# Optimization experiments

Measured on AMD Instinct MI355X. Metric: run time of the kernel, lower is better.

Reference implementation:

```python
import jax, jax.numpy as jnp
import numpy as np

D_IN = 1024
D_OUT = 1024
N_HEADS = 16

def setup_inputs() -> dict:
    key = jax.random.key(0)
    ks = jax.random.split(key, 6)
    s = 0.02
    return {
        "x": jax.random.normal(ks[0], (4, 2048, D_IN), dtype=jnp.float32),
        "Wq": jax.random.normal(ks[1], (D_IN, D_OUT), dtype=jnp.float32) * s,
        "Wk": jax.random.normal(ks[2], (D_IN, D_OUT), dtype=jnp.float32) * s,
        "Wv": jax.random.normal(ks[3], (D_IN, D_OUT), dtype=jnp.float32) * s,
        "Wo": jax.random.normal(ks[4], (D_OUT, D_OUT), dtype=jnp.float32) * s,
        "bo": jax.random.normal(ks[5], (D_OUT,), dtype=jnp.float32) * s,
    }

def reference(x, Wq, Wk, Wv, Wo, bo):
    b, n, _ = x.shape
    hd = D_OUT // N_HEADS
    # project and split heads -> [b, h, n, hd]
    def split(t):
        return t.reshape(b, n, N_HEADS, hd).transpose(0, 2, 1, 3)
    q = split(x @ Wq)
    k = split(x @ Wk)
    v = split(x @ Wv)
    scores = jnp.einsum('bhqd,bhkd->bhqk', q, k)  # [b,h,n,n]
    causal = jnp.tril(jnp.ones((n, n), dtype=bool))
    scores = jnp.where(causal, scores, -jnp.inf)
    attn = jax.nn.softmax(scores / jnp.sqrt(jnp.float32(hd)), axis=-1)
    ctx = jnp.einsum('bhqk,bhkd->bhqd', attn, v)  # [b,h,n,hd]
    ctx = ctx.transpose(0, 2, 1, 3).reshape(b, n, D_OUT)
    return ctx @ Wo + bo
```

## Files before the change

### kernel.cpp

```cpp
#include <hip/hip_runtime.h>
#include <stdint.h>

typedef unsigned short u16;
typedef __attribute__((ext_vector_type(8))) short frag8;
typedef __attribute__((ext_vector_type(4))) float f32x4;
typedef __attribute__((ext_vector_type(4))) unsigned short u16x4;
typedef __attribute__((ext_vector_type(2))) unsigned int u32x2;

#define MFMA_BF16(a,b,c) __builtin_amdgcn_mfma_f32_16x16x32_bf16((a),(b),(c),0,0,0)
#define SMSCALE 0.18033688011112042f
#define EXP2R(x) __builtin_amdgcn_exp2f(x)

__device__ __forceinline__ u16 f2bf(float f) {
  union { float f; uint32_t u; } c; c.f = f;
  uint32_t u = c.u;
  uint32_t r = (u + 0x7fffu + ((u >> 16) & 1u)) >> 16;
  return (u16)r;
}

__device__ __forceinline__ uint32_t pack_bf16(float a, float b) {
  uint32_t au = __float_as_uint(a) + 0x8000u;
  uint32_t bu = __float_as_uint(b) + 0x8000u;
  return __builtin_amdgcn_perm(bu, au, 0x07060302u);
}
__device__ __forceinline__ uint32_t pack_bf16_trunc(float a, float b) {
  return __builtin_amdgcn_perm(__float_as_uint(b), __float_as_uint(a), 0x07060302u);
}

__device__ __forceinline__ void async16(const void* g, void* l) {
  __builtin_amdgcn_global_load_lds((const __attribute__((address_space(1))) void*)g,
                                   (__attribute__((address_space(3))) void*)l,
                                   16, 0, 0);
}

__global__ __launch_bounds__(256) void k_prep(
    const float4* __restrict__ x, u16* __restrict__ xb,
    const float* __restrict__ W0, const float* __restrict__ W1,
    const float* __restrict__ W2, const float* __restrict__ W3,
    u16* __restrict__ D0, u16* __restrict__ D1,
    u16* __restrict__ D2, u16* __restrict__ D3) {
  __shared__ float tile[64][65];
  if (blockIdx.x < 8192) {
    int i = blockIdx.x * 256 + threadIdx.x;
    float4 v = x[i];
    u16x4 o;
    o.x = f2bf(v.x); o.y = f2bf(v.y); o.z = f2bf(v.z); o.w = f2bf(v.w);
    *(u16x4*)(xb + (size_t)i * 4) = o;
    return;
  }
  const int id = blockIdx.x - 8192;
  const int z = id & 3;
  const float* src = (z == 0) ? W0 : (z == 1) ? W1 : (z == 2) ? W2 : W3;
  u16* dst = (z == 0) ? D0 : (z == 1) ? D1 : (z == 2) ? D2 : D3;
  const int bx = ((id >> 2) & 15) * 64;
  const int by = (id >> 6) * 64;
  const int t = threadIdx.x;
  const int tc = (t & 15) * 4;
  const int tr = t >> 4;
  #pragma unroll
  for (int p = 0; p < 4; ++p) {
    int r = tr + p * 16;
    float4 v = *(const float4*)(src + (size_t)(bx + r) * 1024 + by + tc);
    tile[r][tc + 0] = v.x; tile[r][tc + 1] = v.y;
    tile[r][tc + 2] = v.z; tile[r][tc + 3] = v.w;
  }
  __syncthreads();
  #pragma unroll
  for (int p = 0; p < 4; ++p) {
    int r = tr + p * 16;
    u16x4 o;
    o.x = f2bf(tile[tc + 0][r]);
    o.y = f2bf(tile[tc + 1][r]);
    o.z = f2bf(tile[tc + 2][r]);
    o.w = f2bf(tile[tc + 3][r]);
    *(u16x4*)(dst + (size_t)(by + r) * 1024 + bx + tc) = o;
  }
}

__global__ __launch_bounds__(256, 2) void k_gemm_qkv(const u16* __restrict__ xb,
    const u16* __restrict__ Wqt, const u16* __restrict__ Wkt, const u16* __restrict__ Wvt,
    u16* __restrict__ Qg, u16* __restrict__ Kg, u16* __restrict__ Vtg) {
  __shared__ __attribute__((aligned(16))) u16 smem[4 * 128 * 64];
  u16* T = smem;
  const int m0 = blockIdx.x * 128, n0 = blockIdx.y * 128;
  const int t = threadIdx.x, lane = t & 63, wv = t >> 6;
  const int lm = lane & 15, quad = lane >> 4;
  const int wr = wv >> 1, wc = wv & 1;
  f32x4 acc[3][4][4] = {};

  for (int k0 = 0; k0 < 1024; k0 += 64) {
    #pragma unroll
    for (int it = 0; it < 4; ++it) {
      int chunk = it * 256 + t;
      int r = chunk >> 3;
      int sc = ((chunk & 7) ^ (r & 7)) * 8;
      async16(xb + (size_t)(m0 + r) * 1024 + k0 + sc,
              smem + (size_t)(it * 256 + wv * 64) * 8);
    }
    #pragma unroll
    for (int z = 0; z < 3; ++z) {
      const u16* Bt = (z == 0) ? Wqt : (z == 1) ? Wkt : Wvt;
      #pragma unroll
      for (int it = 0; it < 4; ++it) {
        int chunk = it * 256 + t;
        int r = chunk >> 3;
        int sc = ((chunk & 7) ^ (r & 7)) * 8;
        async16(Bt + (size_t)(n0 + r) * 1024 + k0 + sc,
                smem + (size_t)((z + 1) * 1024 + it * 256 + wv * 64) * 8);
      }
    }
    __syncthreads();
    #pragma unroll
    for (int kk = 0; kk < 2; ++kk) {
      frag8 a[4];
      #pragma unroll
      for (int i = 0; i < 4; ++i) {
        int row = wr * 64 + i * 16 + lm;
        a[i] = *(const frag8*)(smem + row * 64 + (((kk * 4 + quad) ^ (row & 7)) * 8));
      }
      #pragma unroll
      for (int z = 0; z < 3; ++z) {
        #pragma unroll
        for (int j = 0; j < 4; ++j) {
          int row = wc * 64 + j * 16 + lm;
          frag8 b = *(const frag8*)(smem + (z + 1) * 8192 + row * 64 +
                                    (((kk * 4 + quad) ^ (row & 7)) * 8));
          #pragma unroll
          for (int i = 0; i < 4; ++i)
            acc[z][i][j] = MFMA_BF16(a[i], b, acc[z][i][j]);
        }
      }
    }
    __syncthreads();
  }

  #pragma unroll
  for (int z = 0; z < 2; ++z) {
    u16* tgt = z ? Kg : Qg;
    const float sc = z ? 1.0f : SMSCALE;
    #pragma unroll
    for (int i = 0; i < 4; ++i)
      #pragma unroll
      for (int j = 0; j < 4; ++j) {
        const int col = n0 + wc * 64 + j * 16 + lm;
        const int h = col >> 6, d = col & 63;
        #pragma unroll
        for (int reg = 0; reg < 4; ++reg) {
          const int row = m0 + wr * 64 + i * 16 + quad * 4 + reg;
          const int bb = row >> 11, nn = row & 2047;
          tgt[(((size_t)bb * 16 + h) * 2048 + nn) * 64 + d] = f2bf(acc[z][i][j][reg] * sc);
        }
      }
  }
  {
    const int bb = m0 >> 11, nn0 = m0 & 2047;
    const int h0 = n0 >> 6;
    #pragma unroll
    for (int p = 0; p < 2; ++p) {
      if (wc == p) {
        #pragma unroll
        for (int i = 0; i < 4; ++i)
          #pragma unroll
          for (int j = 0; j < 4; ++j) {
            const int rT = j * 16 + lm;
            #pragma unroll
            for (int reg = 0; reg < 4; ++reg) {
              const int cT = wr * 64 + i * 16 + quad * 4 + reg;
              T[rT * 136 + cT] = f2bf(acc[2][i][j][reg]);
            }
          }
      }
      __syncthreads();
      #pragma unroll
      for (int cc = 0; cc < 4; ++cc) {
        int chunk = cc * 256 + t;
        int r = chunk >> 4, tk = (chunk & 15) * 8;
        frag8 v = *(const frag8*)(T + r * 136 + tk);
        *(frag8*)(Vtg + (((size_t)bb * 16 + h0 + p) * 64 + r) * 2048 + nn0 + tk) = v;
      }
      __syncthreads();
    }
  }
}

__global__ __launch_bounds__(256, 2) void k_attn(const u16* __restrict__ Qg,
                                                 const u16* __restrict__ Kg,
                                                 const u16* __restrict__ Vtg,
                                                 u16* __restrict__ ctx) {
  __shared__ __attribute__((aligned(16))) u16 Ks[2][64 * 64];
  __shared__ __attribute__((aligned(16))) u16 Vts[2][64 * 64];
  __shared__ __attribute__((aligned(16))) u16 Ps[4 * 16 * 72];
  const int bid = blockIdx.x;
  const int ib = bid >> 6;
  const int bh = ((bid >> 3) & 7) * 8 + (bid & 7);
  const int qts[4] = {2 * ib, 2 * ib + 1, 30 - 2 * ib, 31 - 2 * ib};
  const int t = threadIdx.x, lane = t & 63, wv = t >> 6;
  const int lm = lane & 15, quad = lane >> 4;
  const int b = bh >> 4, h = bh & 15;
  u16* const PsW = Ps + wv * (16 * 72);

  frag8 aq[4][2];
  #pragma unroll
  for (int qa = 0; qa < 4; ++qa) {
    const u16* qp = Qg + ((size_t)bh * 2048 + qts[qa] * 64 + wv * 16 + lm) * 64 + quad * 8;
    aq[qa][0] = *(const frag8*)(qp);
    aq[qa][1] = *(const frag8*)(qp + 32);
  }
  f32x4 o[4][4] = {};
  float l[4] = {0.f, 0.f, 0.f, 0.f};
  const int nst = 32 - 2 * ib;

  const u16* ksrc[2]; const u16* vsrc[2];
  #pragma unroll
  for (int it = 0; it < 2; ++it) {
    int chunk = it * 256 + t;
    int r = chunk >> 3, c = chunk & 7;
    int sc = (c ^ (r & 7)) * 8;
    ksrc[it] = Kg  + ((size_t)bh * 2048 + r) * 64 + sc;
    vsrc[it] = Vtg + ((size_t)bh * 64 + r) * 2048 + sc;
  }
  int offs[8];
  #pragma unroll
  for (int x = 0; x < 4; ++x)
    #pragma unroll
    for (int y = 0; y < 2; ++y)
      offs[x * 2 + y] = (x * 16 + lm) * 64 + (((y * 4 + quad) ^ (lm & 7)) * 8);

  auto stage = [&](int kt, int buf) {
    #pragma unroll
    for (int it = 0; it < 2; ++it) {
      async16(ksrc[it] + (size_t)kt * 4096, &Ks[buf][(it * 256 + wv * 64) * 8]);
      async16(vsrc[it] + (size_t)kt * 64,   &Vts[buf][(it * 256 + wv * 64) * 8]);
    }
  };

  stage(0, 0);
  for (int kt0 = 0; kt0 < nst; ++kt0) {
    const int cur = kt0 & 1;
    __syncthreads();
    if (kt0 + 1 < nst) stage(kt0 + 1, cur ^ 1);

    frag8 kf[8];
    #pragma unroll
    for (int i = 0; i < 8; ++i) kf[i] = *(const frag8*)(&Ks[cur][offs[i]]);

    uint32_t pk[4][8];
    #pragma unroll
    for (int qa = 0; qa < 4; ++qa) {
      if (qts[qa] < kt0) continue;
      f32x4 s[4];
      #pragma unroll
      for (int kt = 0; kt < 4; ++kt) {
        f32x4 z = {0.f, 0.f, 0.f, 0.f};
        z = MFMA_BF16(kf[kt * 2 + 0], aq[qa][0], z);
        z = MFMA_BF16(kf[kt * 2 + 1], aq[qa][1], z);
        s[kt] = z;
      }
      if (kt0 == qts[qa]) {
        #pragma unroll
        for (int kt = 0; kt < 4; ++kt)
          #pragma unroll
          for (int rg = 0; rg < 4; ++rg)
            if (kt * 16 + quad * 4 + rg > wv * 16 + lm) s[kt][rg] = -3.0e38f;
      }
      float rs = 0.f;
      #pragma unroll
      for (int kt = 0; kt < 4; ++kt) {
        float p0 = EXP2R(s[kt][0]);
        float p1 = EXP2R(s[kt][1]);
        float p2 = EXP2R(s[kt][2]);
        float p3 = EXP2R(s[kt][3]);
        rs += (p0 + p1) + (p2 + p3);
        pk[qa][kt * 2 + 0] = pack_bf16_trunc(p0, p1);
        pk[qa][kt * 2 + 1] = pack_bf16_trunc(p2, p3);
      }
      l[qa] += rs;
    }

    frag8 vf[8];
    #pragma unroll
    for (int i = 0; i < 8; ++i) vf[i] = *(const frag8*)(&Vts[cur][offs[i]]);

    #pragma unroll
    for (int qa = 0; qa < 4; ++qa) {
      if (qts[qa] < kt0) continue;
      #pragma unroll
      for (int kt = 0; kt < 4; ++kt) {
        u32x2 w; w.x = pk[qa][kt * 2 + 0]; w.y = pk[qa][kt * 2 + 1];
        *(u32x2*)(PsW + lm * 72 + kt * 16 + quad * 4) = w;
      }
      #pragma unroll
      for (int ks = 0; ks < 2; ++ks) {
        frag8 bp = *(const frag8*)(PsW + lm * 72 + ks * 32 + quad * 8);
        #pragma unroll
        for (int dt = 0; dt < 4; ++dt)
          o[qa][dt] = MFMA_BF16(vf[dt * 2 + ks], bp, o[qa][dt]);
      }
    }
  }

  #pragma unroll
  for (int qa = 0; qa < 4; ++qa) {
    float lv = l[qa];
    lv += __shfl_xor(lv, 16);
    lv += __shfl_xor(lv, 32);
    const float inv = 1.0f / lv;
    #pragma unroll
    for (int dt = 0; dt < 4; ++dt) {
      *(uint32_t*)(PsW + lm * 72 + dt * 16 + quad * 4)     = pack_bf16(o[qa][dt][0] * inv, o[qa][dt][1] * inv);
      *(uint32_t*)(PsW + lm * 72 + dt * 16 + quad * 4 + 2) = pack_bf16(o[qa][dt][2] * inv, o[qa][dt][3] * inv);
    }
    const int rr = lane >> 2, cc = (lane & 3) * 8;
    const size_t row = (size_t)b * 2048 + qts[qa] * 64 + wv * 16 + rr;
    #pragma unroll
    for (int half = 0; half < 2; ++half) {
      frag8 vo = *(const frag8*)(PsW + rr * 72 + cc + half * 32);
      *(frag8*)(ctx + row * 1024 + h * 64 + cc + half * 32) = vo;
    }
  }
}

__global__ __launch_bounds__(256) void k_gemm_out(const u16* __restrict__ ctx,
    const u16* __restrict__ Wot, const float* __restrict__ bo, float* __restrict__ out) {
  __shared__ __attribute__((aligned(16))) u16 As[128 * 64];
  __shared__ __attribute__((aligned(16))) u16 Bs[128 * 64];
  const int m0 = blockIdx.x * 128, n0 = blockIdx.y * 128;
  const int t = threadIdx.x, lane = t & 63, wv = t >> 6;
  const int lm = lane & 15, quad = lane >> 4;
  const int wr = wv >> 1, wc = wv & 1;
  f32x4 acc[4][4] = {};
  for (int k0 = 0; k0 < 1024; k0 += 64) {
    #pragma unroll
    for (int it = 0; it < 4; ++it) {
      int chunk = it * 256 + t;
      int r = chunk >> 3;
      int sc = ((chunk & 7) ^ (r & 7)) * 8;
      async16(ctx + (size_t)(m0 + r) * 1024 + k0 + sc, As + (size_t)(it * 256 + wv * 64) * 8);
      async16(Wot + (size_t)(n0 + r) * 1024 + k0 + sc, Bs + (size_t)(it * 256 + wv * 64) * 8);
    }
    __syncthreads();
    #pragma unroll
    for (int kk = 0; kk < 2; ++kk) {
      frag8 a[4];
      #pragma unroll
      for (int i = 0; i < 4; ++i) {
        int row = wr * 64 + i * 16 + lm;
        a[i] = *(const frag8*)(As + row * 64 + (((kk * 4 + quad) ^ (row & 7)) * 8));
      }
      #pragma unroll
      for (int j = 0; j < 4; ++j) {
        int row = wc * 64 + j * 16 + lm;
        frag8 b = *(const frag8*)(Bs + row * 64 + (((kk * 4 + quad) ^ (row & 7)) * 8));
        #pragma unroll
        for (int i = 0; i < 4; ++i)
          acc[i][j] = MFMA_BF16(a[i], b, acc[i][j]);
      }
    }
    __syncthreads();
  }
  #pragma unroll
  for (int i = 0; i < 4; ++i)
    #pragma unroll
    for (int j = 0; j < 4; ++j) {
      const int col = n0 + wc * 64 + j * 16 + lm;
      const float bias = bo[col];
      #pragma unroll
      for (int reg = 0; reg < 4; ++reg) {
        const int row = m0 + wr * 64 + i * 16 + quad * 4 + reg;
        out[(size_t)row * 1024 + col] = acc[i][j][reg] + bias;
      }
    }
}

extern "C" void kernel_launch(void* const* d_in, const int* in_sizes, int n_in,
                              void* d_out, int out_size, void* d_ws, size_t ws_size,
                              hipStream_t stream) {
  const float* x  = (const float*)d_in[0];
  const float* Wq = (const float*)d_in[1];
  const float* Wk = (const float*)d_in[2];
  const float* Wv = (const float*)d_in[3];
  const float* Wo = (const float*)d_in[4];
  const float* bo = (const float*)d_in[5];
  float* out = (float*)d_out;
  char* ws = (char*)d_ws;

  u16* xb   = (u16*)(ws);
  u16* Wqt  = (u16*)(ws + ((size_t)16 << 20));
  u16* Wkt  = (u16*)(ws + ((size_t)18 << 20));
  u16* Wvt  = (u16*)(ws + ((size_t)20 << 20));
  u16* Wot  = (u16*)(ws + ((size_t)22 << 20));
  u16* Qg   = (u16*)(ws + ((size_t)24 << 20));
  u16* Kg   = (u16*)(ws + ((size_t)40 << 20));
  u16* Vtg  = (u16*)(ws + ((size_t)56 << 20));
  u16* ctxb = (u16*)(ws + ((size_t)72 << 20));

  k_prep<<<9216, 256, 0, stream>>>((const float4*)x, xb, Wq, Wk, Wv, Wo,
                                   Wqt, Wkt, Wvt, Wot);
  k_gemm_qkv<<<dim3(64, 8), 256, 0, stream>>>(xb, Wqt, Wkt, Wvt, Qg, Kg, Vtg);
  k_attn<<<512, 256, 0, stream>>>(Qg, Kg, Vtg, ctxb);
  k_gemm_out<<<dim3(64, 8), 256, 0, stream>>>(ctxb, Wot, bo, out);
}
```

Before: 218.0 us.

## Rewrite QKV GEMM with 256x256 tiles over fused weights and double-buffered pipeline

The QKV projection now treats Wq, Wk and Wv as one contiguous 3072-wide weight matrix, which works because the transposed weights sit back to back in the workspace. It computes 256x256 output tiles with 512 threads, so each block stores only one output kind: Q, K, or transposed V. The K loop uses double-buffered async LDS loads, interleaving prefetch of the next slice with MFMA groups under raised wave priority. This is meant to improve operand reuse and hide global load latency behind compute. The trade-off is fewer, larger blocks and heavier LDS use per block, which may lower occupancy.

```diff
diff --git a/kernel.cpp b/kernel.cpp
--- a/kernel.cpp
+++ b/kernel.cpp
@@ -77,106 +77,170 @@
   }
 }
 
-__global__ __launch_bounds__(256, 2) void k_gemm_qkv(const u16* __restrict__ xb,
-    const u16* __restrict__ Wqt, const u16* __restrict__ Wkt, const u16* __restrict__ Wvt,
+__global__ __launch_bounds__(512, 2) void k_gemm_qkv(
+    const u16* __restrict__ xb, const u16* __restrict__ Wt,
     u16* __restrict__ Qg, u16* __restrict__ Kg, u16* __restrict__ Vtg) {
-  __shared__ __attribute__((aligned(16))) u16 smem[4 * 128 * 64];
-  u16* T = smem;
-  const int m0 = blockIdx.x * 128, n0 = blockIdx.y * 128;
+  __shared__ __attribute__((aligned(16))) u16 smem[65536];
+  const int bid = blockIdx.x;
+  const int mt = bid / 12, nt = bid - mt * 12;
+  const int m0 = mt * 256, n0g = nt * 256;
   const int t = threadIdx.x, lane = t & 63, wv = t >> 6;
   const int lm = lane & 15, quad = lane >> 4;
-  const int wr = wv >> 1, wc = wv & 1;
-  f32x4 acc[3][4][4] = {};
-
-  for (int k0 = 0; k0 < 1024; k0 += 64) {
-    #pragma unroll
-    for (int it = 0; it < 4; ++it) {
-      int chunk = it * 256 + t;
-      int r = chunk >> 3;
-      int sc = ((chunk & 7) ^ (r & 7)) * 8;
-      async16(xb + (size_t)(m0 + r) * 1024 + k0 + sc,
-              smem + (size_t)(it * 256 + wv * 64) * 8);
-    }
-    #pragma unroll
-    for (int z = 0; z < 3; ++z) {
-      const u16* Bt = (z == 0) ? Wqt : (z == 1) ? Wkt : Wvt;
-      #pragma unroll
-      for (int it = 0; it < 4; ++it) {
-        int chunk = it * 256 + t;
-        int r = chunk >> 3;
-        int sc = ((chunk & 7) ^ (r & 7)) * 8;
-        async16(Bt + (size_t)(n0 + r) * 1024 + k0 + sc,
-                smem + (size_t)((z + 1) * 1024 + it * 256 + wv * 64) * 8);
-      }
-    }
-    __syncthreads();
-    #pragma unroll
-    for (int kk = 0; kk < 2; ++kk) {
-      frag8 a[4];
+  const int wr = wv >> 2, wc = wv & 3;
+  f32x4 acc[8][4] = {};
+
+  const u16* Asrc[2]; const u16* Bsrc[2];
+  #pragma unroll
+  for (int it = 0; it < 2; ++it) {
+    int ch = it * 512 + t;
+    int rr = ch >> 2, c = ch & 3;
+    int sw = (c ^ ((rr >> 1) & 3)) * 8;
+    Asrc[it] = xb + (size_t)(m0 + rr) * 1024 + sw;
+    Bsrc[it] = Wt + (size_t)(n0g + rr) * 1024 + sw;
+  }
+  const int dst0 = (wv * 64) * 8, dst1 = (512 + wv * 64) * 8;
+
+  int offA[2][2][4], offB[2][4];
+  #pragma unroll
+  for (int kk = 0; kk < 2; ++kk) {
+    #pragma unroll
+    for (int h = 0; h < 2; ++h)
       #pragma unroll
       for (int i = 0; i < 4; ++i) {
-        int row = wr * 64 + i * 16 + lm;
-        a[i] = *(const frag8*)(smem + row * 64 + (((kk * 4 + quad) ^ (row & 7)) * 8));
-      }
-      #pragma unroll
-      for (int z = 0; z < 3; ++z) {
-        #pragma unroll
-        for (int j = 0; j < 4; ++j) {
-          int row = wc * 64 + j * 16 + lm;
-          frag8 b = *(const frag8*)(smem + (z + 1) * 8192 + row * 64 +
-                                    (((kk * 4 + quad) ^ (row & 7)) * 8));
-          #pragma unroll
-          for (int i = 0; i < 4; ++i)
-            acc[z][i][j] = MFMA_BF16(a[i], b, acc[z][i][j]);
-        }
-      }
-    }
-    __syncthreads();
-  }
-
-  #pragma unroll
-  for (int z = 0; z < 2; ++z) {
+        int rr = wr * 128 + h * 64 + i * 16 + lm;
+        offA[kk][h][i] = kk * 8192 + rr * 32 + ((quad ^ ((rr >> 1) & 3)) * 8);
+      }
+    #pragma unroll
+    for (int j = 0; j < 4; ++j) {
+      int rr = wc * 64 + j * 16 + lm;
+      offB[kk][j] = 16384 + kk * 8192 + rr * 32 + ((quad ^ ((rr >> 1) & 3)) * 8);
+    }
+  }
+
+  auto stageA = [&](int kk, int nb, int kg) {
+    async16(Asrc[0] + kg + kk * 32, smem + nb * 32768 + kk * 8192 + dst0);
+    async16(Asrc[1] + kg + kk * 32, smem + nb * 32768 + kk * 8192 + dst1);
+  };
+  auto stageB = [&](int kk, int nb, int kg) {
+    async16(Bsrc[0] + kg + kk * 32, smem + nb * 32768 + 16384 + kk * 8192 + dst0);
+    async16(Bsrc[1] + kg + kk * 32, smem + nb * 32768 + 16384 + kk * 8192 + dst1);
+  };
+
+  stageA(0, 0, 0); stageB(0, 0, 0); stageA(1, 0, 0); stageB(1, 0, 0);
+  asm volatile("s_waitcnt vmcnt(4)" ::: "memory");
+  __builtin_amdgcn_s_barrier();
+
+  for (int tt = 0; tt < 16; ++tt) {
+    const int buf = (tt & 1) * 32768, nb = (tt + 1) & 1;
+    const int kg = (tt + 1) * 64;
+    const bool pf = (tt + 1 < 16);
+    frag8 a[4], b[4];
+
+    #pragma unroll
+    for (int i = 0; i < 4; ++i) a[i] = *(const frag8*)(smem + buf + offA[0][0][i]);
+    #pragma unroll
+    for (int j = 0; j < 4; ++j) b[j] = *(const frag8*)(smem + buf + offB[0][j]);
+    if (pf) stageA(0, nb, kg);
+    __builtin_amdgcn_s_barrier();
+    __builtin_amdgcn_s_setprio(1);
+    #pragma unroll
+    for (int j = 0; j < 4; ++j)
+      #pragma unroll
+      for (int i = 0; i < 4; ++i)
+        acc[i][j] = MFMA_BF16(a[i], b[j], acc[i][j]);
+    __builtin_amdgcn_s_setprio(0);
+    __builtin_amdgcn_s_barrier();
+
+    #pragma unroll
+    for (int i = 0; i < 4; ++i) a[i] = *(const frag8*)(smem + buf + offA[0][1][i]);
+    if (pf) stageB(0, nb, kg);
+    __builtin_amdgcn_s_barrier();
+    __builtin_amdgcn_s_setprio(1);
+    #pragma unroll
+    for (int j = 0; j < 4; ++j)
+      #pragma unroll
+      for (int i = 0; i < 4; ++i)
+        acc[4 + i][j] = MFMA_BF16(a[i], b[j], acc[4 + i][j]);
+    __builtin_amdgcn_s_setprio(0);
+    if (pf) { asm volatile("s_waitcnt vmcnt(4)" ::: "memory"); }
+    else    { asm volatile("s_waitcnt vmcnt(0)" ::: "memory"); }
+    __builtin_amdgcn_s_barrier();
+
+    #pragma unroll
+    for (int i = 0; i < 4; ++i) a[i] = *(const frag8*)(smem + buf + offA[1][0][i]);
+    #pragma unroll
+    for (int j = 0; j < 4; ++j) b[j] = *(const frag8*)(smem + buf + offB[1][j]);
+    if (pf) stageA(1, nb, kg);
+    __builtin_amdgcn_s_barrier();
+    __builtin_amdgcn_s_setprio(1);
+    #pragma unroll
+    for (int j = 0; j < 4; ++j)
+      #pragma unroll
+      for (int i = 0; i < 4; ++i)
+        acc[i][j] = MFMA_BF16(a[i], b[j], acc[i][j]);
+    __builtin_amdgcn_s_setprio(0);
+    __builtin_amdgcn_s_barrier();
+
+    #pragma unroll
+    for (int i = 0; i < 4; ++i) a[i] = *(const frag8*)(smem + buf + offA[1][1][i]);
+    if (pf) stageB(1, nb, kg);
+    __builtin_amdgcn_s_barrier();
+    __builtin_amdgcn_s_setprio(1);
+    #pragma unroll
+    for (int j = 0; j < 4; ++j)
+      #pragma unroll
+      for (int i = 0; i < 4; ++i)
+        acc[4 + i][j] = MFMA_BF16(a[i], b[j], acc[4 + i][j]);
+    __builtin_amdgcn_s_setprio(0);
+    if (pf) { asm volatile("s_waitcnt vmcnt(4)" ::: "memory"); }
+    else    { asm volatile("s_waitcnt vmcnt(0)" ::: "memory"); }
+    __builtin_amdgcn_s_barrier();
+  }
+
+  const int z = n0g >> 10, nz = n0g & 1023;
+  if (z < 2) {
     u16* tgt = z ? Kg : Qg;
     const float sc = z ? 1.0f : SMSCALE;
     #pragma unroll
-    for (int i = 0; i < 4; ++i)
+    for (int I = 0; I < 8; ++I)
       #pragma unroll
       for (int j = 0; j < 4; ++j) {
-        const int col = n0 + wc * 64 + j * 16 + lm;
-        const int h = col >> 6, d = col & 63;
+        const int col = nz + wc * 64 + j * 16 + lm;
+        const int hh = col >> 6, d = col & 63;
         #pragma unroll
         for (int reg = 0; reg < 4; ++reg) {
-          const int row = m0 + wr * 64 + i * 16 + quad * 4 + reg;
+          const int row = m0 + wr * 128 + (I >> 2) * 64 + (I & 3) * 16 + quad * 4 + reg;
           const int bb = row >> 11, nn = row & 2047;
-          tgt[(((size_t)bb * 16 + h) * 2048 + nn) * 64 + d] = f2bf(acc[z][i][j][reg] * sc);
+          tgt[(((size_t)bb * 16 + hh) * 2048 + nn) * 64 + d] = f2bf(acc[I][j][reg] * sc);
         }
       }
-  }
-  {
-    const int bb = m0 >> 11, nn0 = m0 & 2047;
-    const int h0 = n0 >> 6;
+  } else {
+    u16* T = smem;
+    const int bb = m0 >> 11, nn0 = m0 & 2047, h0 = nz >> 6;
+    __syncthreads();
     #pragma unroll
     for (int p = 0; p < 2; ++p) {
-      if (wc == p) {
+      if (wr == p) {
         #pragma unroll
-        for (int i = 0; i < 4; ++i)
+        for (int I = 0; I < 8; ++I)
           #pragma unroll
           for (int j = 0; j < 4; ++j) {
-            const int rT = j * 16 + lm;
+            const int colL = wc * 64 + j * 16 + lm;
             #pragma unroll
             for (int reg = 0; reg < 4; ++reg) {
-              const int cT = wr * 64 + i * 16 + quad * 4 + reg;
-              T[rT * 136 + cT] = f2bf(acc[2][i][j][reg]);
+              const int tokL = (I >> 2) * 64 + (I & 3) * 16 + quad * 4 + reg;
+              T[colL * 136 + tokL] = f2bf(acc[I][j][reg]);
             }
           }
       }
       __syncthreads();
       #pragma unroll
-      for (int cc = 0; cc < 4; ++cc) {
-        int chunk = cc * 256 + t;
+      for (int cc = 0; cc < 8; ++cc) {
+        int chunk = cc * 512 + t;
         int r = chunk >> 4, tk = (chunk & 15) * 8;
         frag8 v = *(const frag8*)(T + r * 136 + tk);
-        *(frag8*)(Vtg + (((size_t)bb * 16 + h0 + p) * 64 + r) * 2048 + nn0 + tk) = v;
+        *(frag8*)(Vtg + (((size_t)bb * 16 + h0 + (r >> 6)) * 64 + (r & 63)) * 2048 +
+                  nn0 + p * 128 + tk) = v;
       }
       __syncthreads();
     }
@@ -396,7 +460,7 @@
 
   k_prep<<<9216, 256, 0, stream>>>((const float4*)x, xb, Wq, Wk, Wv, Wo,
                                    Wqt, Wkt, Wvt, Wot);
-  k_gemm_qkv<<<dim3(64, 8), 256, 0, stream>>>(xb, Wqt, Wkt, Wvt, Qg, Kg, Vtg);
+  k_gemm_qkv<<<384, 512, 0, stream>>>(xb, Wqt, Qg, Kg, Vtg);
   k_attn<<<512, 256, 0, stream>>>(Qg, Kg, Vtg, ctxb);
   k_gemm_out<<<dim3(64, 8), 256, 0, stream>>>(ctxb, Wot, bo, out);
 }
```

Result: slower. 239.8 us (+10.0%).
